# Optimization experiments

Measured on AMD Instinct MI355X. Metric: run time of the kernel, lower is better.

## Reference

```python
import jax, jax.numpy as jnp
import numpy as np

D, W, B, T = 128, 512, 512, 512

# Tsit5 Butcher tableau (Tsitouras 2011), as used by diffrax.Tsit5
A21 = 0.161
A31, A32 = -0.008480655492356989, 0.335480655492357
A41, A42, A43 = 2.8971530571054935, -6.359448489975075, 4.3622954328695815
A51, A52, A53, A54 = 5.325864828439257, -11.748883564062828, 7.4955393428898365, -0.09249506636175525
A61, A62, A63, A64, A65 = 5.86145544294642, -12.92096931784711, 8.159367898576159, -0.071584973281401, -0.028269050394068383
B1, B2, B3, B4, B5, B6 = 0.09646076681806523, 0.01, 0.4798896504144996, 1.379008574103742, -3.290069515436081, 2.324710524099774


def setup_inputs() -> dict:
    key = jax.random.key(0)
    ks = jax.random.split(key, 8)
    u = lambda k, shape, s: jax.random.uniform(k, shape, minval=-s, maxval=s, dtype=jnp.float32)
    s3 = float(np.sqrt(1.0 / 3.0))
    sD = float(1.0 / np.sqrt(D))
    sW = float(1.0 / np.sqrt(W))
    return {
        "ts": jnp.arange(T, dtype=jnp.float32) * 1e-3,  # uniform save grid, dt0 = 1e-3
        "yi": jax.random.normal(ks[0], (B, 1, D), dtype=jnp.float32),
        "w1": u(ks[1], (W, D), sD), "b1": u(ks[2], (W,), sD),
        "w2": u(ks[3], (W, W), sW), "b2": u(ks[4], (W,), sW),
        "w3": u(ks[5], (D, W), sW), "b3": u(ks[6], (D,), sW),
        "A": u(ks[7], (D, D), s3),
    }


def reference(ts, yi, w1, b1, w2, b2, w3, b3, A):
    # StabilizedFunc: f(y) = MLP(y) + A @ y, batched over B
    def vf(y):  # y: [B, D]
        h = jnp.tanh(y @ w1.T + b1)
        h = jnp.tanh(h @ w2.T + b2)
        return h @ w3.T + b3 + y @ A.T

    def step(y, h):  # one constant-step Tsit5 step of size h
        k1 = vf(y)
        k2 = vf(y + h * (A21 * k1))
        k3 = vf(y + h * (A31 * k1 + A32 * k2))
        k4 = vf(y + h * (A41 * k1 + A42 * k2 + A43 * k3))
        k5 = vf(y + h * (A51 * k1 + A52 * k2 + A53 * k3 + A54 * k4))
        k6 = vf(y + h * (A61 * k1 + A62 * k2 + A63 * k3 + A64 * k4 + A65 * k5))
        y_new = y + h * (B1 * k1 + B2 * k2 + B3 * k3 + B4 * k4 + B5 * k5 + B6 * k6)
        return y_new, y_new

    y0 = yi[:, 0, :]                      # [B, D]
    dts = ts[1:] - ts[:-1]                # [T-1]
    _, ys = jax.lax.scan(step, y0, dts)   # ys: [T-1, B, D]
    out = jnp.concatenate([y0[None], ys], axis=0)  # [T, B, D]
    return jnp.transpose(out, (1, 0, 2))  # [B, T, D]
```

## Files before the change

### kernel.cpp

```cpp
#include <hip/hip_runtime.h>
#include <stdint.h>


#define Dd 128
#define Ww 512
#define Tt 512
#define NSTEP 511
#define NWG 32
#define NTHR 512

#define GRP_USH 1024
#define WAVE_USH (50 * GRP_USH)
#define WS_TOT (8 * WAVE_USH)

#define RING_PER_WAVE 10240
#define H1F 81920
#define H2F 98304
#define Y0F 114688
#define Y1F 118784
#define ATF 122880
#define DTF 123072
#define SMEMB 125120

typedef __attribute__((ext_vector_type(8))) __bf16 bf16x8;
typedef __attribute__((ext_vector_type(4))) float f32x4;

__device__ __forceinline__ unsigned short f2b(float f) {
  union { float f; unsigned int u; } v; v.f = f;
  return (unsigned short)((v.u + 0x7fffu + ((v.u >> 16) & 1u)) >> 16);
}
__device__ __forceinline__ float fast_tanh(float x) {
  x = fminf(fmaxf(x, -15.f), 15.f);
  float e = __expf(2.f * x);
  return (e - 1.f) / (e + 1.f);
}
__device__ __forceinline__ int fragaddr(int m, int n) {
  return ((n >> 5) << 10) + ((((n >> 3) & 3) * 16 + m) << 4) + ((n & 7) << 1);
}

__device__ const float RKC[48] = {
  0.161f, 0.f, 0.f, 0.f, 0.f, 0.f, 0.f, 0.f,
  -0.008480655492356989f, 0.335480655492357f, 0.f, 0.f, 0.f, 0.f, 0.f, 0.f,
  2.8971530571054935f, -6.359448489975075f, 4.3622954328695815f, 0.f, 0.f, 0.f, 0.f, 0.f,
  5.325864828439257f, -11.748883564062828f, 7.4955393428898365f,
  -0.09249506636175525f, 0.f, 0.f, 0.f, 0.f,
  5.86145544294642f, -12.92096931784711f, 8.159367898576159f,
  -0.071584973281401f, -0.028269050394068383f, 0.f, 0.f, 0.f,
  0.09646076681806523f, 0.01f, 0.4798896504144996f, 1.379008574103742f,
  -3.290069515436081f, 2.324710524099774f, 0.f, 0.f
};

#define GLDS(gp, lp) __builtin_amdgcn_global_load_lds( \
    (const __attribute__((address_space(1))) unsigned int*)(const void*)(gp), \
    (__attribute__((address_space(3))) unsigned int*)(void*)(lp), 16, 0, 0)

#define SLOTP(g) (ring_w + (((g) % 5) * 2048))

#define VMW4() do { asm volatile("s_waitcnt vmcnt(4)" ::: "memory"); \
                    __builtin_amdgcn_sched_barrier(0); } while (0)
#define LGKM0() do { asm volatile("s_waitcnt lgkmcnt(0)" ::: "memory"); \
                     __builtin_amdgcn_sched_barrier(0); } while (0)
#define LBAR() do { asm volatile("s_waitcnt lgkmcnt(0)" ::: "memory"); \
                    __builtin_amdgcn_s_barrier(); } while (0)

#define ISSUE(g) do { \
    GLDS(gstream + ((g) << 10) + lsrc,       SLOTP(g)); \
    GLDS(gstream + ((g) << 10) + 512 + lsrc, SLOTP(g) + 1024); } while (0)

#define MFMA(a, b, c) __builtin_amdgcn_mfma_f32_16x16x32_bf16((a), (b), (c), 0, 0, 0)
#define CPK(kd) do { kd[0]=kk[0]; kd[1]=kk[1]; kd[2]=kk[2]; kd[3]=kk[3]; } while (0)

__global__ void prep_kernel(const float* __restrict__ w1,
                            const float* __restrict__ w2,
                            const float* __restrict__ w3,
                            const float* __restrict__ Am,
                            unsigned short* __restrict__ wsb) {
  for (int i = blockIdx.x * blockDim.x + threadIdx.x; i < WS_TOT;
       i += gridDim.x * blockDim.x) {
    const int j    = i & 7;
    const int L    = (i >> 3) & 63;
    const int l16  = L & 15;
    const int q    = L >> 4;
    const int tile = (i >> 9) & 1;
    const int g    = (i >> 10) % 50;
    const int w    = i / WAVE_USH;
    float v;
    if (g < 8) {
      const int nt = (g & 1) * 2 + tile, ks = g >> 1;
      v = w1[(w * 64 + nt * 16 + l16) * Dd + ks * 32 + q * 8 + j];
    } else if (g < 40) {
      const int gg = g - 8;
      const int nt = (gg & 1) * 2 + tile, ks = gg >> 1;
      v = w2[(w * 64 + nt * 16 + l16) * Ww + ks * 32 + q * 8 + j];
    } else if (g < 48) {
      const int kcol = 2 * (g - 40) + tile;
      v = w3[(w * 16 + l16) * Ww + kcol * 32 + q * 8 + j];
    } else {
      const int kcol = 2 * (g - 48) + tile;
      v = Am[(w * 16 + l16) * Dd + kcol * 32 + q * 8 + j];
    }
    wsb[i] = f2b(v);
  }
}

__global__ void __launch_bounds__(NTHR, 1)
ode_kernel(const float* __restrict__ ts,
           const float* __restrict__ yi,
           const float* __restrict__ b1,
           const float* __restrict__ b2,
           const float* __restrict__ b3,
           float* __restrict__ out,
           const unsigned short* __restrict__ wsb)
{
  extern __shared__ char smem_c[];

  const int tid  = threadIdx.x;
  const int wid  = tid >> 6;
  const int lane = tid & 63;
  const int l16  = lane & 15;
  const int quad = lane >> 4;
  const int lob  = lane << 4;
  const int lsrc = lane << 3;
  const int b0   = blockIdx.x * 16;

  char* ring_w = smem_c + wid * RING_PER_WAVE;
  char* h1f = smem_c + H1F;
  char* h2f = smem_c + H2F;

  const unsigned short* gstream = wsb + wid * WAVE_USH;

  if (tid < 48) *(float*)(smem_c + ATF + (tid << 2)) = RKC[tid];
  for (int i = tid; i < NSTEP; i += NTHR)
    *(float*)(smem_c + DTF + (i << 2)) = ts[i + 1] - ts[i];

  float b1v[4], b2v[4];
  #pragma unroll
  for (int nt = 0; nt < 4; ++nt) {
    b1v[nt] = b1[(wid << 6) + (nt << 4) + l16];
    b2v[nt] = b2[(wid << 6) + (nt << 4) + l16];
  }
  const float b3v = b3[(wid << 4) + l16];

  int hwaddr[4];
  #pragma unroll
  for (int nt = 0; nt < 4; ++nt)
    hwaddr[nt] = fragaddr(quad << 2, (wid << 6) + (nt << 4) + l16);
  const int nC = (wid << 4) + l16;
  const int ydst = fragaddr(quad << 2, nC);

  float y[4];
  #pragma unroll
  for (int r = 0; r < 4; ++r) {
    y[r] = yi[(size_t)(b0 + (quad << 2) + r) * Dd + nC];
    *(unsigned short*)(smem_c + Y0F + ydst + (r << 4)) = f2b(y[r]);
    out[(size_t)(b0 + (quad << 2) + r) * (Tt * Dd) + nC] = y[r];
  }

  float k0[4] = {0,0,0,0}, k1[4] = {0,0,0,0}, k2[4] = {0,0,0,0},
        k3[4] = {0,0,0,0}, k4[4] = {0,0,0,0}, k5[4] = {0,0,0,0};

  __syncthreads();

  ISSUE(0); ISSUE(1); ISSUE(2); ISSUE(3);

  #pragma unroll 1
  for (int t = 0; t < NSTEP; ++t) {
    const float hdt = *(const float*)(smem_c + DTF + (t << 2));

    #pragma unroll 1
    for (int s = 0; s < 6; ++s) {
      const char* ybr = smem_c + ((s & 1) ? Y1F : Y0F);
      char*       ybw = smem_c + ((s & 1) ? Y0F : Y1F);

      LBAR();

      {
        f32x4 accA[4];
        #pragma unroll
        for (int nt = 0; nt < 4; ++nt) { f32x4 z = {0.f,0.f,0.f,0.f}; accA[nt] = z; }
        #pragma unroll
        for (int ks = 0; ks < 4; ++ks) {
          VMW4();
          bf16x8 af = *(const bf16x8*)(ybr + (ks << 10) + lob);
          bf16x8 bv[4];
          #pragma unroll
          for (int nt = 0; nt < 4; ++nt)
            bv[nt] = *(const bf16x8*)(SLOTP(2*ks + (nt >> 1)) +
                                      ((nt & 1) << 10) + lob);
          LGKM0();
          if (ks == 0)      { ISSUE(4);  ISSUE(5);  }
          else if (ks == 1) { ISSUE(6);  ISSUE(7);  }
          else if (ks == 2) { ISSUE(8);  ISSUE(9);  }
          else              { ISSUE(10); ISSUE(11); }
          #pragma unroll
          for (int nt = 0; nt < 4; ++nt)
            accA[nt] = MFMA(af, bv[nt], accA[nt]);
        }
        #pragma unroll
        for (int nt = 0; nt < 4; ++nt)
          #pragma unroll
          for (int r = 0; r < 4; ++r)
            *(unsigned short*)(h1f + hwaddr[nt] + (r << 4)) =
                f2b(fast_tanh(accA[nt][r] + b1v[nt]));
      }
      LBAR();

      {
        f32x4 accB[4];
        #pragma unroll
        for (int nt = 0; nt < 4; ++nt) { f32x4 z = {0.f,0.f,0.f,0.f}; accB[nt] = z; }
        #pragma unroll
        for (int ks = 0; ks < 16; ++ks) {
          VMW4();
          bf16x8 af = *(const bf16x8*)(h1f + (ks << 10) + lob);
          bf16x8 bv[4];
          #pragma unroll
          for (int nt = 0; nt < 4; ++nt)
            bv[nt] = *(const bf16x8*)(SLOTP(8 + 2*ks + (nt >> 1)) +
                                      ((nt & 1) << 10) + lob);
          LGKM0();
          if (ks < 14)       { ISSUE(12 + 2*ks); ISSUE(13 + 2*ks); }
          else if (ks == 14) { ISSUE(40); ISSUE(41); }
          else               { ISSUE(42); ISSUE(43); }
          #pragma unroll
          for (int nt = 0; nt < 4; ++nt)
            accB[nt] = MFMA(af, bv[nt], accB[nt]);
        }
        #pragma unroll
        for (int nt = 0; nt < 4; ++nt)
          #pragma unroll
          for (int r = 0; r < 4; ++r)
            *(unsigned short*)(h2f + hwaddr[nt] + (r << 4)) =
                f2b(fast_tanh(accB[nt][r] + b2v[nt]));
      }
      LBAR();

      {
        f32x4 accC0 = {0.f, 0.f, 0.f, 0.f};
        f32x4 accC1 = {0.f, 0.f, 0.f, 0.f};
        #pragma unroll
        for (int cc = 0; cc < 5; ++cc) {
          VMW4();
          bf16x8 afv[4], bv[4];
          #pragma unroll
          for (int t4 = 0; t4 < 4; ++t4) {
            const char* ab = (cc < 4) ? (h2f + ((4*cc + t4) << 10))
                                      : (ybr + (t4 << 10));
            afv[t4] = *(const bf16x8*)(ab + lob);
            bv[t4]  = *(const bf16x8*)(SLOTP(40 + 2*cc + (t4 >> 1)) +
                                       ((t4 & 1) << 10) + lob);
          }
          LGKM0();
          if (cc == 0)      { ISSUE(44); ISSUE(45); }
          else if (cc == 1) { ISSUE(46); ISSUE(47); }
          else if (cc == 2) { ISSUE(48); ISSUE(49); }
          else if (cc == 3) { ISSUE(0);  ISSUE(1);  }
          else              { ISSUE(2);  ISSUE(3);  }
          accC0 = MFMA(afv[0], bv[0], accC0);
          accC1 = MFMA(afv[1], bv[1], accC1);
          accC0 = MFMA(afv[2], bv[2], accC0);
          accC1 = MFMA(afv[3], bv[3], accC1);
        }
        float kk[4];
        #pragma unroll
        for (int r = 0; r < 4; ++r) kk[r] = accC0[r] + accC1[r] + b3v;
        switch (s) {
          case 0: CPK(k0); break;
          case 1: CPK(k1); break;
          case 2: CPK(k2); break;
          case 3: CPK(k3); break;
          case 4: CPK(k4); break;
          default: CPK(k5); break;
        }
      }

      {
        const float* cp = (const float*)(smem_c + ATF + (s << 5));
        const float c0 = cp[0], c1 = cp[1], c2 = cp[2];
        const float c3 = cp[3], c4 = cp[4], c5 = cp[5];
        float a_[4];
        #pragma unroll
        for (int r = 0; r < 4; ++r)
          a_[r] = y[r] + hdt * (c0*k0[r] + c1*k1[r] + c2*k2[r] +
                                c3*k3[r] + c4*k4[r] + c5*k5[r]);
        #pragma unroll
        for (int r = 0; r < 4; ++r)
          *(unsigned short*)(ybw + ydst + (r << 4)) = f2b(a_[r]);
        if (s == 5) {
          #pragma unroll
          for (int r = 0; r < 4; ++r) {
            y[r] = a_[r];
            out[(size_t)(b0 + (quad << 2) + r) * (Tt * Dd) +
                (size_t)(t + 1) * Dd + nC] = a_[r];
          }
        }
      }
    }
  }
}

extern "C" void kernel_launch(void* const* d_in, const int* in_sizes, int n_in,
                              void* d_out, int out_size, void* d_ws, size_t ws_size,
                              hipStream_t stream) {
  (void)in_sizes; (void)n_in; (void)out_size; (void)ws_size;

  const float* ts = (const float*)d_in[0];
  const float* yi = (const float*)d_in[1];
  const float* w1 = (const float*)d_in[2];
  const float* b1 = (const float*)d_in[3];
  const float* w2 = (const float*)d_in[4];
  const float* b2 = (const float*)d_in[5];
  const float* w3 = (const float*)d_in[6];
  const float* b3 = (const float*)d_in[7];
  const float* Am = (const float*)d_in[8];
  float* outp = (float*)d_out;
  unsigned short* wsb = (unsigned short*)d_ws;

  (void)hipFuncSetAttribute(reinterpret_cast<const void*>(ode_kernel),
                            hipFuncAttributeMaxDynamicSharedMemorySize,
                            SMEMB);

  prep_kernel<<<400, 256, 0, stream>>>(w1, w2, w3, Am, wsb);
  ode_kernel<<<dim3(NWG), dim3(NTHR), SMEMB, stream>>>(
      ts, yi, b1, b2, b3, outp, wsb);
}
```

Baseline: 37.06 ms.

## Keep W1 and A fragments in registers and stream only W2/W3 via deeper ring

The small W1 and A weight fragments are now loaded once into registers per wave, and the per-stage streaming ring carries only W2 and W3 tiles. The ring is restructured into three 4 KB slots with four loads per issue, so prefetch runs deeper and uses a uniform wrap-around advance. The intent is to cut global-to-LDS streaming traffic and the waits in the first layer and the linear term. In exchange it adds register pressure (about 20 extra bf16x8 values per lane), enlarges LDS use, and changes the workspace layout produced by the prep kernel.

```diff
diff --git a/kernel.cpp b/kernel.cpp
--- a/kernel.cpp
+++ b/kernel.cpp
@@ -9,18 +9,19 @@
 #define NWG 32
 #define NTHR 512
 
-#define GRP_USH 1024
-#define WAVE_USH (50 * GRP_USH)
-#define WS_TOT (8 * WAVE_USH)
-
-#define RING_PER_WAVE 10240
-#define H1F 81920
-#define H2F 98304
-#define Y0F 114688
-#define Y1F 118784
-#define ATF 122880
-#define DTF 123072
-#define SMEMB 125120
+#define WSTR_W 40960
+#define WSTAT_BASE 327680
+#define WSTAT_W 10240
+#define WS_TOT 409600
+
+#define RING_W_B 12288
+#define H1F 98304
+#define H2F 114688
+#define Y0F 131072
+#define Y1F 135168
+#define ATF 139264
+#define DTF 139520
+#define SMEMB 141568
 
 typedef __attribute__((ext_vector_type(8))) __bf16 bf16x8;
 typedef __attribute__((ext_vector_type(4))) float f32x4;
@@ -54,18 +55,20 @@
     (const __attribute__((address_space(1))) unsigned int*)(const void*)(gp), \
     (__attribute__((address_space(3))) unsigned int*)(void*)(lp), 16, 0, 0)
 
-#define SLOTP(g) (ring_w + (((g) % 5) * 2048))
-
-#define VMW4() do { asm volatile("s_waitcnt vmcnt(4)" ::: "memory"); \
+#define VMW8() do { asm volatile("s_waitcnt vmcnt(8)" ::: "memory"); \
                     __builtin_amdgcn_sched_barrier(0); } while (0)
 #define LGKM0() do { asm volatile("s_waitcnt lgkmcnt(0)" ::: "memory"); \
                      __builtin_amdgcn_sched_barrier(0); } while (0)
 #define LBAR() do { asm volatile("s_waitcnt lgkmcnt(0)" ::: "memory"); \
                     __builtin_amdgcn_s_barrier(); } while (0)
 
-#define ISSUE(g) do { \
-    GLDS(gstream + ((g) << 10) + lsrc,       SLOTP(g)); \
-    GLDS(gstream + ((g) << 10) + 512 + lsrc, SLOTP(g) + 1024); } while (0)
+#define ISSUE4(ro_, igo_) do { \
+    GLDS(gsb + (igo_),        ring_w + (ro_)); \
+    GLDS(gsb + (igo_) + 1024, ring_w + (ro_) + 1024); \
+    GLDS(gsb + (igo_) + 2048, ring_w + (ro_) + 2048); \
+    GLDS(gsb + (igo_) + 3072, ring_w + (ro_) + 3072); } while (0)
+#define ADV() do { ro  = (ro  == 8192)  ? 0 : ro  + 4096; \
+                   igo = (igo == 77824) ? 0 : igo + 4096; } while (0)
 
 #define MFMA(a, b, c) __builtin_amdgcn_mfma_f32_16x16x32_bf16((a), (b), (c), 0, 0, 0)
 #define CPK(kd) do { kd[0]=kk[0]; kd[1]=kk[1]; kd[2]=kk[2]; kd[3]=kk[3]; } while (0)
@@ -77,27 +80,32 @@
                             unsigned short* __restrict__ wsb) {
   for (int i = blockIdx.x * blockDim.x + threadIdx.x; i < WS_TOT;
        i += gridDim.x * blockDim.x) {
-    const int j    = i & 7;
-    const int L    = (i >> 3) & 63;
-    const int l16  = L & 15;
-    const int q    = L >> 4;
-    const int tile = (i >> 9) & 1;
-    const int g    = (i >> 10) % 50;
-    const int w    = i / WAVE_USH;
     float v;
-    if (g < 8) {
-      const int nt = (g & 1) * 2 + tile, ks = g >> 1;
-      v = w1[(w * 64 + nt * 16 + l16) * Dd + ks * 32 + q * 8 + j];
-    } else if (g < 40) {
-      const int gg = g - 8;
-      const int nt = (gg & 1) * 2 + tile, ks = gg >> 1;
-      v = w2[(w * 64 + nt * 16 + l16) * Ww + ks * 32 + q * 8 + j];
-    } else if (g < 48) {
-      const int kcol = 2 * (g - 40) + tile;
-      v = w3[(w * 16 + l16) * Ww + kcol * 32 + q * 8 + j];
+    if (i < WSTAT_BASE) {
+      const int w = i / WSTR_W, r = i % WSTR_W;
+      const int g = r >> 10, tile = (r >> 9) & 1;
+      const int L = (r >> 3) & 63, j = r & 7;
+      const int l16 = L & 15, q = L >> 4;
+      if (g < 32) {
+        const int nt = (g & 1) * 2 + tile, ks = g >> 1;
+        v = w2[(w * 64 + nt * 16 + l16) * Ww + ks * 32 + q * 8 + j];
+      } else {
+        const int kcol = 2 * (g - 32) + tile;
+        v = w3[(w * 16 + l16) * Ww + kcol * 32 + q * 8 + j];
+      }
     } else {
-      const int kcol = 2 * (g - 48) + tile;
-      v = Am[(w * 16 + l16) * Dd + kcol * 32 + q * 8 + j];
+      const int ii = i - WSTAT_BASE;
+      const int w = ii / WSTAT_W, r = ii % WSTAT_W;
+      const int idx = r >> 10, tile = (r >> 9) & 1;
+      const int L = (r >> 3) & 63, j = r & 7;
+      const int l16 = L & 15, q = L >> 4;
+      if (idx < 8) {
+        const int ks = idx >> 1, nt = (idx & 1) * 2 + tile;
+        v = w1[(w * 64 + nt * 16 + l16) * Dd + ks * 32 + q * 8 + j];
+      } else {
+        const int kcol = 2 * (idx - 8) + tile;
+        v = Am[(w * 16 + l16) * Dd + kcol * 32 + q * 8 + j];
+      }
     }
     wsb[i] = f2b(v);
   }
@@ -120,14 +128,27 @@
   const int l16  = lane & 15;
   const int quad = lane >> 4;
   const int lob  = lane << 4;
-  const int lsrc = lane << 3;
   const int b0   = blockIdx.x * 16;
 
-  char* ring_w = smem_c + wid * RING_PER_WAVE;
+  char* ring_w = smem_c + wid * RING_W_B;
   char* h1f = smem_c + H1F;
   char* h2f = smem_c + H2F;
 
-  const unsigned short* gstream = wsb + wid * WAVE_USH;
+  const char* gsb = (const char*)(wsb + wid * WSTR_W) + (lane << 4);
+  const unsigned short* wstat = wsb + WSTAT_BASE + wid * WSTAT_W;
+
+  bf16x8 w1f[4][4];
+  #pragma unroll
+  for (int ks = 0; ks < 4; ++ks)
+    #pragma unroll
+    for (int nt = 0; nt < 4; ++nt)
+      w1f[ks][nt] = *(const bf16x8*)(wstat + (2*ks + (nt>>1)) * 1024 +
+                                     (nt & 1) * 512 + (lane << 3));
+  bf16x8 Af[4];
+  #pragma unroll
+  for (int kc = 0; kc < 4; ++kc)
+    Af[kc] = *(const bf16x8*)(wstat + 8192 + (kc>>1) * 1024 +
+                              (kc & 1) * 512 + (lane << 3));
 
   if (tid < 48) *(float*)(smem_c + ATF + (tid << 2)) = RKC[tid];
   for (int i = tid; i < NSTEP; i += NTHR)
@@ -161,7 +182,8 @@
 
   __syncthreads();
 
-  ISSUE(0); ISSUE(1); ISSUE(2); ISSUE(3);
+  int ro = 0, igo = 12288;
+  ISSUE4(0, 0); ISSUE4(4096, 4096); ISSUE4(8192, 8192);
 
   #pragma unroll 1
   for (int t = 0; t < NSTEP; ++t) {
@@ -180,21 +202,10 @@
         for (int nt = 0; nt < 4; ++nt) { f32x4 z = {0.f,0.f,0.f,0.f}; accA[nt] = z; }
         #pragma unroll
         for (int ks = 0; ks < 4; ++ks) {
-          VMW4();
           bf16x8 af = *(const bf16x8*)(ybr + (ks << 10) + lob);
-          bf16x8 bv[4];
           #pragma unroll
           for (int nt = 0; nt < 4; ++nt)
-            bv[nt] = *(const bf16x8*)(SLOTP(2*ks + (nt >> 1)) +
-                                      ((nt & 1) << 10) + lob);
-          LGKM0();
-          if (ks == 0)      { ISSUE(4);  ISSUE(5);  }
-          else if (ks == 1) { ISSUE(6);  ISSUE(7);  }
-          else if (ks == 2) { ISSUE(8);  ISSUE(9);  }
-          else              { ISSUE(10); ISSUE(11); }
-          #pragma unroll
-          for (int nt = 0; nt < 4; ++nt)
-            accA[nt] = MFMA(af, bv[nt], accA[nt]);
+            accA[nt] = MFMA(af, w1f[ks][nt], accA[nt]);
         }
         #pragma unroll
         for (int nt = 0; nt < 4; ++nt)
@@ -211,17 +222,15 @@
         for (int nt = 0; nt < 4; ++nt) { f32x4 z = {0.f,0.f,0.f,0.f}; accB[nt] = z; }
         #pragma unroll
         for (int ks = 0; ks < 16; ++ks) {
-          VMW4();
+          VMW8();
           bf16x8 af = *(const bf16x8*)(h1f + (ks << 10) + lob);
           bf16x8 bv[4];
           #pragma unroll
           for (int nt = 0; nt < 4; ++nt)
-            bv[nt] = *(const bf16x8*)(SLOTP(8 + 2*ks + (nt >> 1)) +
-                                      ((nt & 1) << 10) + lob);
+            bv[nt] = *(const bf16x8*)(ring_w + ro + (nt << 10) + lob);
           LGKM0();
-          if (ks < 14)       { ISSUE(12 + 2*ks); ISSUE(13 + 2*ks); }
-          else if (ks == 14) { ISSUE(40); ISSUE(41); }
-          else               { ISSUE(42); ISSUE(43); }
+          ISSUE4(ro, igo);
+          ADV();
           #pragma unroll
           for (int nt = 0; nt < 4; ++nt)
             accB[nt] = MFMA(af, bv[nt], accB[nt]);
@@ -239,27 +248,27 @@
         f32x4 accC0 = {0.f, 0.f, 0.f, 0.f};
         f32x4 accC1 = {0.f, 0.f, 0.f, 0.f};
         #pragma unroll
-        for (int cc = 0; cc < 5; ++cc) {
-          VMW4();
+        for (int cc = 0; cc < 4; ++cc) {
+          VMW8();
           bf16x8 afv[4], bv[4];
           #pragma unroll
           for (int t4 = 0; t4 < 4; ++t4) {
-            const char* ab = (cc < 4) ? (h2f + ((4*cc + t4) << 10))
-                                      : (ybr + (t4 << 10));
-            afv[t4] = *(const bf16x8*)(ab + lob);
-            bv[t4]  = *(const bf16x8*)(SLOTP(40 + 2*cc + (t4 >> 1)) +
-                                       ((t4 & 1) << 10) + lob);
+            afv[t4] = *(const bf16x8*)(h2f + ((4*cc + t4) << 10) + lob);
+            bv[t4]  = *(const bf16x8*)(ring_w + ro + (t4 << 10) + lob);
           }
           LGKM0();
-          if (cc == 0)      { ISSUE(44); ISSUE(45); }
-          else if (cc == 1) { ISSUE(46); ISSUE(47); }
-          else if (cc == 2) { ISSUE(48); ISSUE(49); }
-          else if (cc == 3) { ISSUE(0);  ISSUE(1);  }
-          else              { ISSUE(2);  ISSUE(3);  }
+          ISSUE4(ro, igo);
+          ADV();
           accC0 = MFMA(afv[0], bv[0], accC0);
           accC1 = MFMA(afv[1], bv[1], accC1);
           accC0 = MFMA(afv[2], bv[2], accC0);
           accC1 = MFMA(afv[3], bv[3], accC1);
+        }
+        #pragma unroll
+        for (int kc = 0; kc < 4; ++kc) {
+          bf16x8 afy = *(const bf16x8*)(ybr + (kc << 10) + lob);
+          if (kc & 1) accC1 = MFMA(afy, Af[kc], accC1);
+          else        accC0 = MFMA(afy, Af[kc], accC0);
         }
         float kk[4];
         #pragma unroll
```

New measurement: 37.11 ms. No clear change (+0.1%).

## Stream weight fragments directly into a register ring instead of LDS

Applied to the files above, without the earlier changes.

Replaces the per-wave global-to-LDS weight ring (global_load_lds plus LDS reads of the B operands) with inline-asm global_load_dwordx4 straight into a five-stage register ring of bf16x8 fragments. Loads are waited on with a manual vmcnt(12) instead of separate vmcnt and lgkmcnt waits. This removes the LDS round trip and the lgkm stalls on the weight operand, and shrinks the LDS footprint. In exchange it costs about 80 extra VGPRs. The hand-counted vmcnt is fragile: the compiler does not track when these asm loads complete, and the global output stores also count toward vmcnt.

```diff
diff --git a/kernel.cpp b/kernel.cpp
--- a/kernel.cpp
+++ b/kernel.cpp
@@ -13,14 +13,13 @@
 #define WAVE_USH (50 * GRP_USH)
 #define WS_TOT (8 * WAVE_USH)
 
-#define RING_PER_WAVE 10240
-#define H1F 81920
-#define H2F 98304
-#define Y0F 114688
-#define Y1F 118784
-#define ATF 122880
-#define DTF 123072
-#define SMEMB 125120
+#define H1F 0
+#define H2F 16384
+#define Y0F 32768
+#define Y1F 36864
+#define ATF 40960
+#define DTF 41152
+#define SMEMB 43200
 
 typedef __attribute__((ext_vector_type(8))) __bf16 bf16x8;
 typedef __attribute__((ext_vector_type(4))) float f32x4;
@@ -50,22 +49,20 @@
   -3.290069515436081f, 2.324710524099774f, 0.f, 0.f
 };
 
-#define GLDS(gp, lp) __builtin_amdgcn_global_load_lds( \
-    (const __attribute__((address_space(1))) unsigned int*)(const void*)(gp), \
-    (__attribute__((address_space(3))) unsigned int*)(void*)(lp), 16, 0, 0)
-
-#define SLOTP(g) (ring_w + (((g) % 5) * 2048))
-
-#define VMW4() do { asm volatile("s_waitcnt vmcnt(4)" ::: "memory"); \
-                    __builtin_amdgcn_sched_barrier(0); } while (0)
-#define LGKM0() do { asm volatile("s_waitcnt lgkmcnt(0)" ::: "memory"); \
+#define LDG1(dst, off_) \
+  asm volatile("global_load_dwordx4 %0, %1, off" \
+               : "=&v"(dst) : "v"(gsb + (off_)))
+
+#define ISSUE_ITER(bi, mm) do { \
+    LDG1(bb[bi][0], (((mm) % 25) * 4096)); \
+    LDG1(bb[bi][1], (((mm) % 25) * 4096 + 1024)); \
+    LDG1(bb[bi][2], (((mm) % 25) * 4096 + 2048)); \
+    LDG1(bb[bi][3], (((mm) % 25) * 4096 + 3072)); } while (0)
+
+#define VMW12() do { asm volatile("s_waitcnt vmcnt(12)" ::: "memory"); \
                      __builtin_amdgcn_sched_barrier(0); } while (0)
 #define LBAR() do { asm volatile("s_waitcnt lgkmcnt(0)" ::: "memory"); \
                     __builtin_amdgcn_s_barrier(); } while (0)
-
-#define ISSUE(g) do { \
-    GLDS(gstream + ((g) << 10) + lsrc,       SLOTP(g)); \
-    GLDS(gstream + ((g) << 10) + 512 + lsrc, SLOTP(g) + 1024); } while (0)
 
 #define MFMA(a, b, c) __builtin_amdgcn_mfma_f32_16x16x32_bf16((a), (b), (c), 0, 0, 0)
 #define CPK(kd) do { kd[0]=kk[0]; kd[1]=kk[1]; kd[2]=kk[2]; kd[3]=kk[3]; } while (0)
@@ -120,14 +117,12 @@
   const int l16  = lane & 15;
   const int quad = lane >> 4;
   const int lob  = lane << 4;
-  const int lsrc = lane << 3;
   const int b0   = blockIdx.x * 16;
 
-  char* ring_w = smem_c + wid * RING_PER_WAVE;
   char* h1f = smem_c + H1F;
   char* h2f = smem_c + H2F;
 
-  const unsigned short* gstream = wsb + wid * WAVE_USH;
+  const char* gsb = (const char*)(wsb + wid * WAVE_USH) + lob;
 
   if (tid < 48) *(float*)(smem_c + ATF + (tid << 2)) = RKC[tid];
   for (int i = tid; i < NSTEP; i += NTHR)
@@ -161,7 +156,8 @@
 
   __syncthreads();
 
-  ISSUE(0); ISSUE(1); ISSUE(2); ISSUE(3);
+  bf16x8 bb[5][4];
+  ISSUE_ITER(0, 0); ISSUE_ITER(1, 1); ISSUE_ITER(2, 2); ISSUE_ITER(3, 3);
 
   #pragma unroll 1
   for (int t = 0; t < NSTEP; ++t) {
@@ -179,22 +175,13 @@
         #pragma unroll
         for (int nt = 0; nt < 4; ++nt) { f32x4 z = {0.f,0.f,0.f,0.f}; accA[nt] = z; }
         #pragma unroll
-        for (int ks = 0; ks < 4; ++ks) {
-          VMW4();
-          bf16x8 af = *(const bf16x8*)(ybr + (ks << 10) + lob);
-          bf16x8 bv[4];
+        for (int m = 0; m < 4; ++m) {
+          VMW12();
+          bf16x8 af = *(const bf16x8*)(ybr + (m << 10) + lob);
+          ISSUE_ITER((m + 4) % 5, m + 4);
           #pragma unroll
           for (int nt = 0; nt < 4; ++nt)
-            bv[nt] = *(const bf16x8*)(SLOTP(2*ks + (nt >> 1)) +
-                                      ((nt & 1) << 10) + lob);
-          LGKM0();
-          if (ks == 0)      { ISSUE(4);  ISSUE(5);  }
-          else if (ks == 1) { ISSUE(6);  ISSUE(7);  }
-          else if (ks == 2) { ISSUE(8);  ISSUE(9);  }
-          else              { ISSUE(10); ISSUE(11); }
-          #pragma unroll
-          for (int nt = 0; nt < 4; ++nt)
-            accA[nt] = MFMA(af, bv[nt], accA[nt]);
+            accA[nt] = MFMA(af, bb[m][nt], accA[nt]);
         }
         #pragma unroll
         for (int nt = 0; nt < 4; ++nt)
@@ -211,20 +198,12 @@
         for (int nt = 0; nt < 4; ++nt) { f32x4 z = {0.f,0.f,0.f,0.f}; accB[nt] = z; }
         #pragma unroll
         for (int ks = 0; ks < 16; ++ks) {
-          VMW4();
+          VMW12();
           bf16x8 af = *(const bf16x8*)(h1f + (ks << 10) + lob);
-          bf16x8 bv[4];
+          ISSUE_ITER((ks + 8) % 5, ks + 8);
           #pragma unroll
           for (int nt = 0; nt < 4; ++nt)
-            bv[nt] = *(const bf16x8*)(SLOTP(8 + 2*ks + (nt >> 1)) +
-                                      ((nt & 1) << 10) + lob);
-          LGKM0();
-          if (ks < 14)       { ISSUE(12 + 2*ks); ISSUE(13 + 2*ks); }
-          else if (ks == 14) { ISSUE(40); ISSUE(41); }
-          else               { ISSUE(42); ISSUE(43); }
-          #pragma unroll
-          for (int nt = 0; nt < 4; ++nt)
-            accB[nt] = MFMA(af, bv[nt], accB[nt]);
+            accB[nt] = MFMA(af, bb[(ks + 4) % 5][nt], accB[nt]);
         }
         #pragma unroll
         for (int nt = 0; nt < 4; ++nt)
@@ -240,26 +219,24 @@
         f32x4 accC1 = {0.f, 0.f, 0.f, 0.f};
         #pragma unroll
         for (int cc = 0; cc < 5; ++cc) {
-          VMW4();
-          bf16x8 afv[4], bv[4];
-          #pragma unroll
-          for (int t4 = 0; t4 < 4; ++t4) {
-            const char* ab = (cc < 4) ? (h2f + ((4*cc + t4) << 10))
-                                      : (ybr + (t4 << 10));
-            afv[t4] = *(const bf16x8*)(ab + lob);
-            bv[t4]  = *(const bf16x8*)(SLOTP(40 + 2*cc + (t4 >> 1)) +
-                                       ((t4 & 1) << 10) + lob);
+          VMW12();
+          bf16x8 a0, a1, a2, a3;
+          if (cc < 4) {
+            a0 = *(const bf16x8*)(h2f + ((4*cc + 0) << 10) + lob);
+            a1 = *(const bf16x8*)(h2f + ((4*cc + 1) << 10) + lob);
+            a2 = *(const bf16x8*)(h2f + ((4*cc + 2) << 10) + lob);
+            a3 = *(const bf16x8*)(h2f + ((4*cc + 3) << 10) + lob);
+          } else {
+            a0 = *(const bf16x8*)(ybr + (0 << 10) + lob);
+            a1 = *(const bf16x8*)(ybr + (1 << 10) + lob);
+            a2 = *(const bf16x8*)(ybr + (2 << 10) + lob);
+            a3 = *(const bf16x8*)(ybr + (3 << 10) + lob);
           }
-          LGKM0();
-          if (cc == 0)      { ISSUE(44); ISSUE(45); }
-          else if (cc == 1) { ISSUE(46); ISSUE(47); }
-          else if (cc == 2) { ISSUE(48); ISSUE(49); }
-          else if (cc == 3) { ISSUE(0);  ISSUE(1);  }
-          else              { ISSUE(2);  ISSUE(3);  }
-          accC0 = MFMA(afv[0], bv[0], accC0);
-          accC1 = MFMA(afv[1], bv[1], accC1);
-          accC0 = MFMA(afv[2], bv[2], accC0);
-          accC1 = MFMA(afv[3], bv[3], accC1);
+          ISSUE_ITER((cc + 24) % 5, cc + 24);
+          accC0 = MFMA(a0, bb[cc][0], accC0);
+          accC1 = MFMA(a1, bb[cc][1], accC1);
+          accC0 = MFMA(a2, bb[cc][2], accC0);
+          accC1 = MFMA(a3, bb[cc][3], accC1);
         }
         float kk[4];
         #pragma unroll
@@ -297,6 +274,8 @@
       }
     }
   }
+
+  asm volatile("s_waitcnt vmcnt(0) lgkmcnt(0)" ::: "memory");
 }
 
 extern "C" void kernel_launch(void* const* d_in, const int* in_sizes, int n_in,
```

After: 42.52 ms. 1.15x slower.
